# Kernel tuning notes

Measured on AMD Instinct MI355X. Metric: run time of the kernel, lower is better.

Reference implementation:

```python
import jax, jax.numpy as jnp
import numpy as np

B, S, D = 8, 512, 256
H, DH = 8, 32          # attention_heads, head_dim = 256/8
NB = 8                 # n_attention_blocks
COMP = 128             # compressed_features_size
LN_EPS = 1e-5


def _layernorm(x, g, b):
    mu = jnp.mean(x, axis=-1, keepdims=True)
    var = jnp.var(x, axis=-1, keepdims=True)
    return (x - mu) * jax.lax.rsqrt(var + LN_EPS) * g + b


def setup_inputs() -> dict:
    key = jax.random.key(0)
    ks = jax.random.split(key, 16)
    sc = 0.02
    d = {
        "state": jax.random.normal(ks[0], (B, S, 1, 64, 64), jnp.float32),
        "fc1_w": jax.random.normal(ks[1], (4096, 4096), jnp.float32) * sc,
        "fc1_b": jnp.zeros((4096,), jnp.float32),
        "fc2_w": jax.random.normal(ks[2], (4096, 2048), jnp.float32) * sc,
        "fc2_b": jnp.zeros((2048,), jnp.float32),
        "fc3_w": jax.random.normal(ks[3], (2048, 1024), jnp.float32) * sc,
        "fc3_b": jnp.zeros((1024,), jnp.float32),
        "fc4_w": jax.random.normal(ks[4], (1024, 512), jnp.float32) * sc,
        "fc4_b": jnp.zeros((512,), jnp.float32),
        "fc5_w": jax.random.normal(ks[5], (512, D), jnp.float32) * sc,
        "fc5_b": jnp.zeros((D,), jnp.float32),
        "pre_w": jax.random.normal(ks[6], (D, D), jnp.float32) * sc,
        "pre_b": jnp.zeros((D,), jnp.float32),
        "pos_w": jax.random.normal(ks[7], (1, S, D), jnp.float32) * sc,
        "enc_w": jax.random.normal(ks[8], (NB, D, 3 * D), jnp.float32) * sc,
        "enc_b": jnp.zeros((NB, 3 * D), jnp.float32),
        "ln1_g": jnp.ones((NB, D), jnp.float32),
        "ln1_b": jnp.zeros((NB, D), jnp.float32),
        "ln2_g": jnp.ones((NB, D), jnp.float32),
        "ln2_b": jnp.zeros((NB, D), jnp.float32),
        "res_w1": jax.random.normal(ks[9], (NB, D, 4 * D), jnp.float32) * sc,
        "res_b1": jnp.zeros((NB, 4 * D), jnp.float32),
        "res_w2": jax.random.normal(ks[10], (NB, 4 * D, D), jnp.float32) * sc,
        "res_b2": jnp.zeros((NB, D), jnp.float32),
        "out_w": jax.random.normal(ks[11], (D, COMP), jnp.float32) * sc,
        "out_b": jnp.zeros((COMP,), jnp.float32),
    }
    return d


def _forward(state, fc1_w, fc1_b, fc2_w, fc2_b, fc3_w, fc3_b, fc4_w, fc4_b,
             fc5_w, fc5_b, pre_w, pre_b, pos_w, enc_w, enc_b,
             ln1_g, ln1_b, ln2_g, ln2_b, res_w1, res_b1, res_w2, res_b2,
             out_w, out_b):
    x = state.reshape(B, S, -1)                       # [B,S,4096]
    x = jax.nn.relu(x @ fc1_w + fc1_b)
    x = jax.nn.relu(x @ fc2_w + fc2_b)
    x = jax.nn.relu(x @ fc3_w + fc3_b)
    x = jax.nn.relu(x @ fc4_w + fc4_b)
    x = jnp.tanh(x @ fc5_w + fc5_b)                   # [B,S,256]
    x = x @ pre_w + pre_b
    x = x + pos_w                                     # positional (dropout off / eval)

    i = jnp.arange(S)[:, None]
    j = jnp.arange(S)[None, :]
    m = (i >= j).astype(jnp.float32)[None, None]      # causal mask [1,1,S,S]
    scale = jax.lax.rsqrt(jnp.float32(DH))

    for l in range(NB):
        xn = _layernorm(x, ln1_g[l], ln1_b[l])
        c = xn @ enc_w[l] + enc_b[l]                  # [B,S,3D]
        q, k, v = jnp.split(c, 3, axis=2)
        q = q.reshape(B, S, H, DH).transpose(0, 2, 1, 3)  # [B,H,S,DH]
        k = k.reshape(B, S, H, DH).transpose(0, 2, 1, 3)
        v = v.reshape(B, S, H, DH).transpose(0, 2, 1, 3)
        w = jnp.einsum("bhqd,bhkd->bhqk", q, k) * scale
        w = w * m - 1e10 * (1.0 - m)
        s = jax.nn.softmax(w, axis=3)
        a = jnp.einsum("bhqk,bhkd->bhqd", s, v)
        a = a.transpose(0, 2, 1, 3).reshape(B, S, D)
        x = x + a
        x = _layernorm(x, ln2_g[l], ln2_b[l])
        h = jax.nn.gelu(x @ res_w1[l] + res_b1[l], approximate=False)
        h = h @ res_w2[l] + res_b2[l]
        x = x + h

    enc = x @ out_w + out_b                           # [B,S,128]
    enc = (enc - jnp.mean(enc)) / jnp.std(enc, ddof=1) + 1e-10
    return enc


def reference(state, fc1_w, fc1_b, fc2_w, fc2_b, fc3_w, fc3_b, fc4_w, fc4_b,
              fc5_w, fc5_b, pre_w, pre_b, pos_w, enc_w, enc_b,
              ln1_g, ln1_b, ln2_g, ln2_b, res_w1, res_b1, res_w2, res_b2,
              out_w, out_b):
    return _forward(state, fc1_w, fc1_b, fc2_w, fc2_b, fc3_w, fc3_b, fc4_w,
                    fc4_b, fc5_w, fc5_b, pre_w, pre_b, pos_w, enc_w, enc_b,
                    ln1_g, ln1_b, ln2_g, ln2_b, res_w1, res_b1, res_w2,
                    res_b2, out_w, out_b)
```

## Files before the change

### kernel.cpp

```cpp
#include <hip/hip_runtime.h>

typedef _Float16 half8 __attribute__((ext_vector_type(8)));
typedef _Float16 half4v __attribute__((ext_vector_type(4)));
typedef _Float16 half2v __attribute__((ext_vector_type(2)));
typedef float f32x4 __attribute__((ext_vector_type(4)));

__device__ __forceinline__ void gload16(const _Float16* g, _Float16* l) {
  __builtin_amdgcn_global_load_lds((const __attribute__((address_space(1))) void*)g,
                                   (__attribute__((address_space(3))) void*)l, 16, 0, 0);
}

__global__ __launch_bounds__(256) void cast_k(const float* __restrict__ in,
                                              _Float16* __restrict__ out, int n) {
  int i = (blockIdx.x * 256 + threadIdx.x) << 2;
  if (i < n) {
    float4 v = *(const float4*)(in + i);
    half4v h;
    h[0] = (_Float16)v.x; h[1] = (_Float16)v.y; h[2] = (_Float16)v.z; h[3] = (_Float16)v.w;
    *(half4v*)(out + i) = h;
  }
}

__global__ __launch_bounds__(256) void tcast_k(const float* __restrict__ W,
                                               _Float16* __restrict__ WT, int K, int N) {
  __shared__ float tile[32][33];
  const size_t zo = (size_t)blockIdx.z * K * N;
  const int n0 = blockIdx.x << 5, k0 = blockIdx.y << 5;
  const int tx = threadIdx.x & 31, ty = threadIdx.x >> 5;
#pragma unroll
  for (int i = 0; i < 4; i++)
    tile[ty + i * 8][tx] = W[zo + (size_t)(k0 + ty + i * 8) * N + n0 + tx];
  __syncthreads();
#pragma unroll
  for (int i = 0; i < 4; i++)
    WT[zo + (size_t)(n0 + ty + i * 8) * K + k0 + tx] = (_Float16)tile[tx][ty + i * 8];
}

template <int BM, int BN, int WGM, int WGN, int MODE>
__global__ __launch_bounds__(256) void gemm_nt(const _Float16* __restrict__ A,
                                               const _Float16* __restrict__ Bt,
                                               const float* __restrict__ bias,
                                               _Float16* __restrict__ outH,
                                               float* __restrict__ outF,
                                               const float* __restrict__ aux,
                                               int M, int N, int K) {
  constexpr int BK = 64;
  constexpr int TM = BM / WGM, TN = BN / WGN;
  constexpr int AM = TM / 16, AN = TN / 16;
  constexpr int LA = BM * BK / 2048, LB = BN * BK / 2048;
  __shared__ __align__(16) _Float16 As[BM * BK];
  __shared__ __align__(16) _Float16 Bs[BN * BK];
  const int tid = threadIdx.x;
  const int lane = tid & 63, w = tid >> 6;
  const int wr = (w / WGN) * TM, wc = (w % WGN) * TN;
  const int lr = lane & 15, quad = lane >> 4;
  const int mb = blockIdx.y * BM, nb = blockIdx.x * BN;

  const _Float16* ga[LA];
  const _Float16* gb[LB];
  _Float16* la[LA];
  _Float16* lb[LB];
#pragma unroll
  for (int i = 0; i < LA; i++) {
    const int c = tid + i * 256, row = c >> 3, j = c & 7;
    ga[i] = A + (size_t)(mb + row) * K + ((j ^ (row & 7)) << 3);
    la[i] = As + c * 8;
  }
#pragma unroll
  for (int i = 0; i < LB; i++) {
    const int c = tid + i * 256, row = c >> 3, j = c & 7;
    gb[i] = Bt + (size_t)(nb + row) * K + ((j ^ (row & 7)) << 3);
    lb[i] = Bs + c * 8;
  }

  f32x4 acc[AM][AN] = {};

  for (int k0 = 0; k0 < K; k0 += BK) {
#pragma unroll
    for (int i = 0; i < LA; i++) gload16(ga[i] + k0, la[i]);
#pragma unroll
    for (int i = 0; i < LB; i++) gload16(gb[i] + k0, lb[i]);
    __syncthreads();
#pragma unroll
    for (int ks = 0; ks < 2; ks++) {
      const int pc = (((ks << 2) | quad) ^ (lane & 7)) << 3;
      half8 af[AM], bf[AN];
#pragma unroll
      for (int mt = 0; mt < AM; mt++)
        af[mt] = *(const half8*)(As + (wr + mt * 16 + lr) * BK + pc);
#pragma unroll
      for (int nt = 0; nt < AN; nt++)
        bf[nt] = *(const half8*)(Bs + (wc + nt * 16 + lr) * BK + pc);
#pragma unroll
      for (int mt = 0; mt < AM; mt++)
#pragma unroll
        for (int nt = 0; nt < AN; nt++)
          acc[mt][nt] = __builtin_amdgcn_mfma_f32_16x16x32_f16(af[mt], bf[nt], acc[mt][nt], 0, 0, 0);
    }
    __syncthreads();
  }

#pragma unroll
  for (int nt = 0; nt < AN; nt++) {
    const int col = nb + wc + (nt << 4) + lr;
    const float bv = bias[col];
#pragma unroll
    for (int mt = 0; mt < AM; mt++) {
      const int row0 = mb + wr + (mt << 4) + (quad << 2);
#pragma unroll
      for (int r = 0; r < 4; r++) {
        const int row = row0 + r;
        const size_t off = (size_t)row * N + col;
        float v = acc[mt][nt][r] + bv;
        if (MODE == 0) {
          outH[off] = (_Float16)fmaxf(v, 0.0f);
        } else if (MODE == 1) {
          outH[off] = (_Float16)tanhf(v);
        } else if (MODE == 2) {
          outH[off] = (_Float16)v;
        } else if (MODE == 3) {
          outF[off] = v + aux[(size_t)(row & 511) * N + col];
        } else if (MODE == 4) {
          outH[off] = (_Float16)(0.5f * v * (1.0f + erff(v * 0.70710678118654752f)));
        } else if (MODE == 5) {
          float xv = aux[off] + v;
          outF[off] = xv;
          outH[off] = (_Float16)xv;
        } else {
          outF[off] = v;
        }
      }
    }
  }
}

__global__ __launch_bounds__(256) void ln_k(const float* __restrict__ x,
                                            const float* __restrict__ g,
                                            const float* __restrict__ b,
                                            _Float16* __restrict__ xn) {
  const int w = threadIdx.x >> 6, lane = threadIdx.x & 63;
  const int row = (blockIdx.x << 2) + w;
  const size_t base = ((size_t)row << 8) + (lane << 2);
  float4 v = *(const float4*)(x + base);
  float s = v.x + v.y + v.z + v.w;
  float sq = v.x * v.x + v.y * v.y + v.z * v.z + v.w * v.w;
#pragma unroll
  for (int o = 32; o; o >>= 1) { s += __shfl_xor(s, o); sq += __shfl_xor(sq, o); }
  const float mean = s * 0.00390625f;
  const float rs = rsqrtf(sq * 0.00390625f - mean * mean + 1e-5f);
  const int c = lane << 2;
  float4 gv = *(const float4*)(g + c);
  float4 bv = *(const float4*)(b + c);
  half4v o4;
  o4[0] = (_Float16)((v.x - mean) * rs * gv.x + bv.x);
  o4[1] = (_Float16)((v.y - mean) * rs * gv.y + bv.y);
  o4[2] = (_Float16)((v.z - mean) * rs * gv.z + bv.z);
  o4[3] = (_Float16)((v.w - mean) * rs * gv.w + bv.w);
  *(half4v*)(xn + base) = o4;
}

__global__ __launch_bounds__(256) void add_ln_k(const float* __restrict__ x,
                                                const float* __restrict__ a,
                                                const float* __restrict__ g,
                                                const float* __restrict__ b,
                                                float* __restrict__ xo,
                                                _Float16* __restrict__ xn) {
  const int w = threadIdx.x >> 6, lane = threadIdx.x & 63;
  const int row = (blockIdx.x << 2) + w;
  const size_t base = ((size_t)row << 8) + (lane << 2);
  float4 v = *(const float4*)(x + base);
  float4 av = *(const float4*)(a + base);
  v.x += av.x; v.y += av.y; v.z += av.z; v.w += av.w;
  float s = v.x + v.y + v.z + v.w;
  float sq = v.x * v.x + v.y * v.y + v.z * v.z + v.w * v.w;
#pragma unroll
  for (int o = 32; o; o >>= 1) { s += __shfl_xor(s, o); sq += __shfl_xor(sq, o); }
  const float mean = s * 0.00390625f;
  const float rs = rsqrtf(sq * 0.00390625f - mean * mean + 1e-5f);
  const int c = lane << 2;
  float4 gv = *(const float4*)(g + c);
  float4 bv = *(const float4*)(b + c);
  float4 o4;
  o4.x = (v.x - mean) * rs * gv.x + bv.x;
  o4.y = (v.y - mean) * rs * gv.y + bv.y;
  o4.z = (v.z - mean) * rs * gv.z + bv.z;
  o4.w = (v.w - mean) * rs * gv.w + bv.w;
  *(float4*)(xo + base) = o4;
  half4v h;
  h[0] = (_Float16)o4.x; h[1] = (_Float16)o4.y; h[2] = (_Float16)o4.z; h[3] = (_Float16)o4.w;
  *(half4v*)(xn + base) = h;
}

__global__ __launch_bounds__(256) void attn_k(const _Float16* __restrict__ qkv,
                                              float* __restrict__ aout) {
  __shared__ __align__(16) char smem[65536];
  _Float16* Ks = (_Float16*)smem;
  _Float16* Vs = (_Float16*)(smem + 32768);
  float* Om = (float*)smem;
  float* Ol = (float*)(smem + 768);
  float* Os = (float*)(smem + 1536);

  const int bid = blockIdx.x;
  const int qt = 7 - (bid & 7), h = (bid >> 3) & 7, b = bid >> 6;
  const int q0 = qt << 6;
  const int t = threadIdx.x, p = t >> 6, tr = t & 63, q = q0 + tr;
  const int nkt = qt + 1;
  const size_t rowbase = (size_t)(b * 512) * 768;

  const half2v* q2 = (const half2v*)(qkv + rowbase + (size_t)q * 768 + h * 32);
  half2v qh[16];
#pragma unroll
  for (int i = 0; i < 16; i++) qh[i] = q2[i];

  for (int c = t; c < nkt * 256; c += 256) {
    const int row = c >> 2, off = (c & 3) << 3;
    const _Float16* kp = qkv + rowbase + (size_t)row * 768 + 256 + h * 32 + off;
    gload16(kp, Ks + c * 8);
    gload16(kp + 256, Vs + c * 8);
  }
  __syncthreads();

  float O[32];
#pragma unroll
  for (int d = 0; d < 32; d++) O[d] = 0.0f;
  float m = -1e30f, lsum = 0.0f;

  for (int kt = p; kt < nkt; kt += 4) {
    const int kb = kt << 6;
    const int rows = (kt == qt) ? (tr + 1) : 64;
    for (int j0 = 0; j0 < rows; j0 += 8) {
      float s[8];
      float mx = -1e30f;
#pragma unroll
      for (int jj = 0; jj < 8; jj++) {
        const half2v* kr = (const half2v*)(Ks + (size_t)(kb + j0 + jj) * 32);
        float a0 = 0.0f, a1 = 0.0f;
#pragma unroll
        for (int d = 0; d < 8; d++) {
          a0 = __builtin_amdgcn_fdot2(qh[d], kr[d], a0, false);
          a1 = __builtin_amdgcn_fdot2(qh[d + 8], kr[d + 8], a1, false);
        }
        const float sc = (a0 + a1) * 0.17677669529663687f;
        s[jj] = (kb + j0 + jj <= q) ? sc : -1e30f;
        mx = fmaxf(mx, s[jj]);
      }
      const float mn = fmaxf(m, mx);
      const float corr = __expf(m - mn);
      lsum *= corr;
#pragma unroll
      for (int d = 0; d < 32; d++) O[d] *= corr;
      m = mn;
#pragma unroll
      for (int jj = 0; jj < 8; jj++) {
        const float pw = __expf(s[jj] - m);
        lsum += pw;
        const half8* vr = (const half8*)(Vs + (size_t)(kb + j0 + jj) * 32);
#pragma unroll
        for (int i = 0; i < 4; i++) {
          half8 vv = vr[i];
#pragma unroll
          for (int d = 0; d < 8; d++) O[i * 8 + d] = fmaf(pw, (float)vv[d], O[i * 8 + d]);
        }
      }
    }
  }

  __syncthreads();
  if (p > 0) {
    Om[(p - 1) * 64 + tr] = m;
    Ol[(p - 1) * 64 + tr] = lsum;
    float* od = Os + ((p - 1) * 64 + tr) * 33;
#pragma unroll
    for (int d = 0; d < 32; d++) od[d] = O[d];
  }
  __syncthreads();
  if (p == 0) {
    float mn = m;
#pragma unroll
    for (int pp = 0; pp < 3; pp++) mn = fmaxf(mn, Om[pp * 64 + tr]);
    const float c0 = __expf(m - mn);
    float lt = lsum * c0;
    float cs[3];
#pragma unroll
    for (int pp = 0; pp < 3; pp++) {
      cs[pp] = __expf(Om[pp * 64 + tr] - mn);
      lt += Ol[pp * 64 + tr] * cs[pp];
    }
    const float inv = 1.0f / lt;
    float* op = aout + ((size_t)(b * 512 + q)) * 256 + h * 32;
#pragma unroll
    for (int d = 0; d < 32; d++) {
      float v = O[d] * c0;
#pragma unroll
      for (int pp = 0; pp < 3; pp++) v += Os[(pp * 64 + tr) * 33 + d] * cs[pp];
      op[d] = v * inv;
    }
  }
}

__global__ __launch_bounds__(256) void reduce_stats_k(const float4* __restrict__ v, int n4,
                                                      float* __restrict__ stats) {
  float s = 0.0f, sq = 0.0f;
  for (int i = blockIdx.x * 256 + threadIdx.x; i < n4; i += gridDim.x * 256) {
    float4 x = v[i];
    s += x.x + x.y + x.z + x.w;
    sq += x.x * x.x + x.y * x.y + x.z * x.z + x.w * x.w;
  }
#pragma unroll
  for (int o = 32; o; o >>= 1) { s += __shfl_xor(s, o); sq += __shfl_xor(sq, o); }
  __shared__ float ss[4], sqq[4];
  const int w = threadIdx.x >> 6;
  if ((threadIdx.x & 63) == 0) { ss[w] = s; sqq[w] = sq; }
  __syncthreads();
  if (threadIdx.x == 0) {
    atomicAdd(&stats[0], ss[0] + ss[1] + ss[2] + ss[3]);
    atomicAdd(&stats[1], sqq[0] + sqq[1] + sqq[2] + sqq[3]);
  }
}

__global__ __launch_bounds__(256) void finalize_k(const float4* __restrict__ enc,
                                                  const float* __restrict__ stats,
                                                  float4* __restrict__ out, int n4, float n) {
  const int i = blockIdx.x * 256 + threadIdx.x;
  if (i >= n4) return;
  const float s = stats[0], q = stats[1];
  const float mean = s / n;
  const float var = (q - s * s / n) / (n - 1.0f);
  const float inv = rsqrtf(var);
  float4 x = enc[i];
  float4 o;
  o.x = (x.x - mean) * inv + 1e-10f;
  o.y = (x.y - mean) * inv + 1e-10f;
  o.z = (x.z - mean) * inv + 1e-10f;
  o.w = (x.w - mean) * inv + 1e-10f;
  out[i] = o;
}

extern "C" void kernel_launch(void* const* d_in, const int* in_sizes, int n_in,
                              void* d_out, int out_size, void* d_ws, size_t ws_size,
                              hipStream_t stream) {
  const float* state = (const float*)d_in[0];
  const float* fc1_w = (const float*)d_in[1];
  const float* fc1_b = (const float*)d_in[2];
  const float* fc2_w = (const float*)d_in[3];
  const float* fc2_b = (const float*)d_in[4];
  const float* fc3_w = (const float*)d_in[5];
  const float* fc3_b = (const float*)d_in[6];
  const float* fc4_w = (const float*)d_in[7];
  const float* fc4_b = (const float*)d_in[8];
  const float* fc5_w = (const float*)d_in[9];
  const float* fc5_b = (const float*)d_in[10];
  const float* pre_w = (const float*)d_in[11];
  const float* pre_b = (const float*)d_in[12];
  const float* pos_w = (const float*)d_in[13];
  const float* enc_w = (const float*)d_in[14];
  const float* enc_b = (const float*)d_in[15];
  const float* ln1_g = (const float*)d_in[16];
  const float* ln1_b = (const float*)d_in[17];
  const float* ln2_g = (const float*)d_in[18];
  const float* ln2_b = (const float*)d_in[19];
  const float* res_w1 = (const float*)d_in[20];
  const float* res_b1 = (const float*)d_in[21];
  const float* res_w2 = (const float*)d_in[22];
  const float* res_b2 = (const float*)d_in[23];
  const float* out_w = (const float*)d_in[24];
  const float* out_b = (const float*)d_in[25];

  char* ws = (char*)d_ws;
  _Float16* wbuf = (_Float16*)ws;
  _Float16* bufA = (_Float16*)(ws + 33554432);
  _Float16* bufB = (_Float16*)(ws + 67108864);
  _Float16* xn16 = bufA;
  _Float16* qkv16 = bufA + 1048576;
  _Float16* h16 = bufA + 4194304;
  _Float16* x16 = bufA + 8388608;
  float* xres = (float*)(ws + 67108864 + 4194304);
  float* aout = xres + 1048576;
  float* enc32 = aout + 1048576;
  float* stats = enc32 + 524288;
  _Float16* encT = (_Float16*)(ws + 67108864 + 16777216);
  _Float16* res1T = encT + 1572864;
  _Float16* res2T = res1T + 2097152;
  _Float16* outT = res2T + 2097152;

  const dim3 tb(256);

  cast_k<<<16384, tb, 0, stream>>>(state, bufA, 16777216);
  tcast_k<<<dim3(128, 128, 1), tb, 0, stream>>>(fc1_w, wbuf, 4096, 4096);
  gemm_nt<128, 128, 2, 2, 0><<<dim3(32, 32), tb, 0, stream>>>(bufA, wbuf, fc1_b, bufB, nullptr, nullptr, 4096, 4096, 4096);
  tcast_k<<<dim3(64, 128, 1), tb, 0, stream>>>(fc2_w, wbuf, 4096, 2048);
  gemm_nt<128, 128, 2, 2, 0><<<dim3(16, 32), tb, 0, stream>>>(bufB, wbuf, fc2_b, bufA, nullptr, nullptr, 4096, 2048, 4096);
  tcast_k<<<dim3(32, 64, 1), tb, 0, stream>>>(fc3_w, wbuf, 2048, 1024);
  gemm_nt<128, 128, 2, 2, 0><<<dim3(8, 32), tb, 0, stream>>>(bufA, wbuf, fc3_b, bufB, nullptr, nullptr, 4096, 1024, 2048);
  tcast_k<<<dim3(16, 32, 1), tb, 0, stream>>>(fc4_w, wbuf, 1024, 512);
  gemm_nt<128, 64, 4, 1, 0><<<dim3(8, 32), tb, 0, stream>>>(bufB, wbuf, fc4_b, bufA, nullptr, nullptr, 4096, 512, 1024);
  tcast_k<<<dim3(8, 16, 1), tb, 0, stream>>>(fc5_w, wbuf, 512, 256);
  gemm_nt<64, 64, 2, 2, 1><<<dim3(4, 64), tb, 0, stream>>>(bufA, wbuf, fc5_b, bufB, nullptr, nullptr, 4096, 256, 512);
  tcast_k<<<dim3(8, 8, 1), tb, 0, stream>>>(pre_w, wbuf, 256, 256);
  gemm_nt<64, 64, 2, 2, 3><<<dim3(4, 64), tb, 0, stream>>>(bufB, wbuf, pre_b, nullptr, xres, pos_w, 4096, 256, 256);

  tcast_k<<<dim3(24, 8, 8), tb, 0, stream>>>(enc_w, encT, 256, 768);
  tcast_k<<<dim3(32, 8, 8), tb, 0, stream>>>(res_w1, res1T, 256, 1024);
  tcast_k<<<dim3(8, 32, 8), tb, 0, stream>>>(res_w2, res2T, 1024, 256);
  tcast_k<<<dim3(4, 8, 1), tb, 0, stream>>>(out_w, outT, 256, 128);

  for (int l = 0; l < 8; l++) {
    ln_k<<<1024, tb, 0, stream>>>(xres, ln1_g + l * 256, ln1_b + l * 256, xn16);
    gemm_nt<128, 64, 4, 1, 2><<<dim3(12, 32), tb, 0, stream>>>(xn16, encT + (size_t)l * 196608, enc_b + l * 768,
                                                               qkv16, nullptr, nullptr, 4096, 768, 256);
    attn_k<<<512, tb, 0, stream>>>(qkv16, aout);
    add_ln_k<<<1024, tb, 0, stream>>>(xres, aout, ln2_g + l * 256, ln2_b + l * 256, xres, xn16);
    gemm_nt<128, 128, 2, 2, 4><<<dim3(8, 32), tb, 0, stream>>>(xn16, res1T + (size_t)l * 262144, res_b1 + l * 1024,
                                                               h16, nullptr, nullptr, 4096, 1024, 256);
    gemm_nt<64, 64, 2, 2, 5><<<dim3(4, 64), tb, 0, stream>>>(h16, res2T + (size_t)l * 262144, res_b2 + l * 256,
                                                             x16, xres, xres, 4096, 256, 1024);
  }

  gemm_nt<64, 64, 2, 2, 6><<<dim3(2, 64), tb, 0, stream>>>(x16, outT, out_b, nullptr, enc32, nullptr, 4096, 128, 256);
  hipMemsetAsync(stats, 0, 2 * sizeof(float), stream);
  reduce_stats_k<<<256, tb, 0, stream>>>((const float4*)enc32, 131072, stats);
  finalize_k<<<512, tb, 0, stream>>>((const float4*)enc32, stats, (float4*)d_out, 131072, 524288.0f);
}
```

Baseline: 1.438 ms.

## Fuse layernorms into GEMMs, merge weight casts, fold stats into output GEMM

Replaces the separate ln_k and add_ln_k kernels with a gemm_ln kernel that computes the (residual add +) layernorm of a 64-row tile in registers, writes fp16 into LDS, and runs the K=256 GEMM directly. The residual buffer is ping-ponged so the fused kernel can write the normalized residual while other blocks still read the old one. The four transformer weight transpose-casts are merged into one launch, the global mean/std reduction is folded into the final GEMM via atomics, and BK is made a template parameter with new tile shapes for the fc3–fc5, pre and res2 GEMMs. Each gemm_ln block recomputes the layernorm for its rows (once per column block), trading extra reads for fewer launches and round trips.

Measured after the change: 1.719 ms. 1.2x slower.

```diff
diff --git a/kernel.cpp b/kernel.cpp
--- a/kernel.cpp
+++ b/kernel.cpp
@@ -21,30 +21,61 @@
   }
 }
 
+__device__ __forceinline__ void tcast_core(const float* __restrict__ W,
+                                           _Float16* __restrict__ WT, int K, int N,
+                                           int n0, int k0, float tile[32][33]) {
+  const int tx = threadIdx.x & 31, ty = threadIdx.x >> 5;
+#pragma unroll
+  for (int i = 0; i < 4; i++)
+    tile[ty + i * 8][tx] = W[(size_t)(k0 + ty + i * 8) * N + n0 + tx];
+  __syncthreads();
+#pragma unroll
+  for (int i = 0; i < 4; i++)
+    WT[(size_t)(n0 + ty + i * 8) * K + k0 + tx] = (_Float16)tile[tx][ty + i * 8];
+}
+
 __global__ __launch_bounds__(256) void tcast_k(const float* __restrict__ W,
                                                _Float16* __restrict__ WT, int K, int N) {
   __shared__ float tile[32][33];
-  const size_t zo = (size_t)blockIdx.z * K * N;
-  const int n0 = blockIdx.x << 5, k0 = blockIdx.y << 5;
-  const int tx = threadIdx.x & 31, ty = threadIdx.x >> 5;
-#pragma unroll
-  for (int i = 0; i < 4; i++)
-    tile[ty + i * 8][tx] = W[zo + (size_t)(k0 + ty + i * 8) * N + n0 + tx];
-  __syncthreads();
-#pragma unroll
-  for (int i = 0; i < 4; i++)
-    WT[zo + (size_t)(n0 + ty + i * 8) * K + k0 + tx] = (_Float16)tile[tx][ty + i * 8];
-}
-
-template <int BM, int BN, int WGM, int WGN, int MODE>
+  tcast_core(W, WT, K, N, blockIdx.x << 5, blockIdx.y << 5, tile);
+}
+
+__global__ __launch_bounds__(256) void tcast_all(const float* __restrict__ enc_w, _Float16* encT,
+                                                 const float* __restrict__ res_w1, _Float16* res1T,
+                                                 const float* __restrict__ res_w2, _Float16* res2T,
+                                                 const float* __restrict__ out_w, _Float16* outT) {
+  __shared__ float tile[32][33];
+  int bid = blockIdx.x;
+  if (bid < 1536) {
+    const int z = bid / 192, r = bid % 192;
+    tcast_core(enc_w + (size_t)z * 196608, encT + (size_t)z * 196608, 256, 768,
+               (r % 24) << 5, (r / 24) << 5, tile);
+  } else if (bid < 3584) {
+    bid -= 1536;
+    const int z = bid / 256, r = bid % 256;
+    tcast_core(res_w1 + (size_t)z * 262144, res1T + (size_t)z * 262144, 256, 1024,
+               (r % 32) << 5, (r / 32) << 5, tile);
+  } else if (bid < 5632) {
+    bid -= 3584;
+    const int z = bid / 256, r = bid % 256;
+    tcast_core(res_w2 + (size_t)z * 262144, res2T + (size_t)z * 262144, 1024, 256,
+               (r % 8) << 5, (r / 8) << 5, tile);
+  } else {
+    bid -= 5632;
+    tcast_core(out_w, outT, 256, 128, (bid % 4) << 5, (bid / 4) << 5, tile);
+  }
+}
+
+template <int BM, int BN, int BK, int WGM, int WGN, int MODE>
 __global__ __launch_bounds__(256) void gemm_nt(const _Float16* __restrict__ A,
                                                const _Float16* __restrict__ Bt,
                                                const float* __restrict__ bias,
                                                _Float16* __restrict__ outH,
                                                float* __restrict__ outF,
                                                const float* __restrict__ aux,
+                                               float* __restrict__ stats,
                                                int M, int N, int K) {
-  constexpr int BK = 64;
+  constexpr int CPR = BK / 8;
   constexpr int TM = BM / WGM, TN = BN / WGN;
   constexpr int AM = TM / 16, AN = TN / 16;
   constexpr int LA = BM * BK / 2048, LB = BN * BK / 2048;
@@ -62,13 +93,13 @@
   _Float16* lb[LB];
 #pragma unroll
   for (int i = 0; i < LA; i++) {
-    const int c = tid + i * 256, row = c >> 3, j = c & 7;
+    const int c = tid + i * 256, row = c / CPR, j = c % CPR;
     ga[i] = A + (size_t)(mb + row) * K + ((j ^ (row & 7)) << 3);
     la[i] = As + c * 8;
   }
 #pragma unroll
   for (int i = 0; i < LB; i++) {
-    const int c = tid + i * 256, row = c >> 3, j = c & 7;
+    const int c = tid + i * 256, row = c / CPR, j = c % CPR;
     gb[i] = Bt + (size_t)(nb + row) * K + ((j ^ (row & 7)) << 3);
     lb[i] = Bs + c * 8;
   }
@@ -82,7 +113,7 @@
     for (int i = 0; i < LB; i++) gload16(gb[i] + k0, lb[i]);
     __syncthreads();
 #pragma unroll
-    for (int ks = 0; ks < 2; ks++) {
+    for (int ks = 0; ks < BK / 32; ks++) {
       const int pc = (((ks << 2) | quad) ^ (lane & 7)) << 3;
       half8 af[AM], bf[AN];
 #pragma unroll
@@ -100,6 +131,7 @@
     __syncthreads();
   }
 
+  float ls = 0.0f, lsq = 0.0f;
 #pragma unroll
   for (int nt = 0; nt < AN; nt++) {
     const int col = nb + wc + (nt << 4) + lr;
@@ -128,67 +160,128 @@
           outH[off] = (_Float16)xv;
         } else {
           outF[off] = v;
+          if (MODE == 7) { ls += v; lsq += v * v; }
         }
       }
     }
   }
-}
-
-__global__ __launch_bounds__(256) void ln_k(const float* __restrict__ x,
-                                            const float* __restrict__ g,
-                                            const float* __restrict__ b,
-                                            _Float16* __restrict__ xn) {
-  const int w = threadIdx.x >> 6, lane = threadIdx.x & 63;
-  const int row = (blockIdx.x << 2) + w;
-  const size_t base = ((size_t)row << 8) + (lane << 2);
-  float4 v = *(const float4*)(x + base);
-  float s = v.x + v.y + v.z + v.w;
-  float sq = v.x * v.x + v.y * v.y + v.z * v.z + v.w * v.w;
-#pragma unroll
-  for (int o = 32; o; o >>= 1) { s += __shfl_xor(s, o); sq += __shfl_xor(sq, o); }
-  const float mean = s * 0.00390625f;
-  const float rs = rsqrtf(sq * 0.00390625f - mean * mean + 1e-5f);
-  const int c = lane << 2;
-  float4 gv = *(const float4*)(g + c);
-  float4 bv = *(const float4*)(b + c);
-  half4v o4;
-  o4[0] = (_Float16)((v.x - mean) * rs * gv.x + bv.x);
-  o4[1] = (_Float16)((v.y - mean) * rs * gv.y + bv.y);
-  o4[2] = (_Float16)((v.z - mean) * rs * gv.z + bv.z);
-  o4[3] = (_Float16)((v.w - mean) * rs * gv.w + bv.w);
-  *(half4v*)(xn + base) = o4;
-}
-
-__global__ __launch_bounds__(256) void add_ln_k(const float* __restrict__ x,
-                                                const float* __restrict__ a,
-                                                const float* __restrict__ g,
-                                                const float* __restrict__ b,
-                                                float* __restrict__ xo,
-                                                _Float16* __restrict__ xn) {
-  const int w = threadIdx.x >> 6, lane = threadIdx.x & 63;
-  const int row = (blockIdx.x << 2) + w;
-  const size_t base = ((size_t)row << 8) + (lane << 2);
-  float4 v = *(const float4*)(x + base);
-  float4 av = *(const float4*)(a + base);
-  v.x += av.x; v.y += av.y; v.z += av.z; v.w += av.w;
-  float s = v.x + v.y + v.z + v.w;
-  float sq = v.x * v.x + v.y * v.y + v.z * v.z + v.w * v.w;
-#pragma unroll
-  for (int o = 32; o; o >>= 1) { s += __shfl_xor(s, o); sq += __shfl_xor(sq, o); }
-  const float mean = s * 0.00390625f;
-  const float rs = rsqrtf(sq * 0.00390625f - mean * mean + 1e-5f);
-  const int c = lane << 2;
-  float4 gv = *(const float4*)(g + c);
-  float4 bv = *(const float4*)(b + c);
-  float4 o4;
-  o4.x = (v.x - mean) * rs * gv.x + bv.x;
-  o4.y = (v.y - mean) * rs * gv.y + bv.y;
-  o4.z = (v.z - mean) * rs * gv.z + bv.z;
-  o4.w = (v.w - mean) * rs * gv.w + bv.w;
-  *(float4*)(xo + base) = o4;
-  half4v h;
-  h[0] = (_Float16)o4.x; h[1] = (_Float16)o4.y; h[2] = (_Float16)o4.z; h[3] = (_Float16)o4.w;
-  *(half4v*)(xn + base) = h;
+  if (MODE == 7) {
+#pragma unroll
+    for (int o = 32; o; o >>= 1) { ls += __shfl_xor(ls, o); lsq += __shfl_xor(lsq, o); }
+    if (lane == 0) {
+      atomicAdd(&stats[0], ls);
+      atomicAdd(&stats[1], lsq);
+    }
+  }
+}
+
+template <int MODE, bool ADD>
+__global__ __launch_bounds__(256) void gemm_ln(const float* __restrict__ X,
+                                               const float* __restrict__ Aadd,
+                                               const float* __restrict__ lng,
+                                               const float* __restrict__ lnb,
+                                               const _Float16* __restrict__ Bt,
+                                               const float* __restrict__ bias,
+                                               _Float16* __restrict__ outH,
+                                               float* __restrict__ xout, int N) {
+  __shared__ __align__(16) _Float16 As[64 * 256];
+  __shared__ __align__(16) _Float16 Bs[64 * 256];
+  const int tid = threadIdx.x;
+  const int lane = tid & 63, w = tid >> 6;
+  const int wr = (w >> 1) << 5, wc = (w & 1) << 5;
+  const int lr = lane & 15, quad = lane >> 4;
+  const int mb = blockIdx.y << 6, nb = blockIdx.x << 6;
+
+#pragma unroll
+  for (int i = 0; i < 8; i++) {
+    const int c = tid + i * 256, row = c >> 5, j = c & 31;
+    gload16(Bt + (size_t)(nb + row) * 256 + ((j ^ (row & 7)) << 3), Bs + c * 8);
+  }
+
+  const int r = tid >> 2, qq = tid & 3;
+  float vals[64];
+  {
+    const float4* xp = (const float4*)(X + ((size_t)(mb + r) << 8) + (qq << 6));
+    const float4* ap = (const float4*)(Aadd + ((size_t)(mb + r) << 8) + (qq << 6));
+    float s = 0.0f, sq = 0.0f;
+#pragma unroll
+    for (int i = 0; i < 16; i++) {
+      float4 v = xp[i];
+      if (ADD) {
+        float4 a = ap[i];
+        v.x += a.x; v.y += a.y; v.z += a.z; v.w += a.w;
+      }
+      vals[i * 4 + 0] = v.x; vals[i * 4 + 1] = v.y; vals[i * 4 + 2] = v.z; vals[i * 4 + 3] = v.w;
+      s += v.x + v.y + v.z + v.w;
+      sq += v.x * v.x + v.y * v.y + v.z * v.z + v.w * v.w;
+    }
+    s += __shfl_xor(s, 1); s += __shfl_xor(s, 2);
+    sq += __shfl_xor(sq, 1); sq += __shfl_xor(sq, 2);
+    const float mean = s * 0.00390625f;
+    const float rs = rsqrtf(sq * 0.00390625f - mean * mean + 1e-5f);
+    const float4* g4 = (const float4*)(lng + (qq << 6));
+    const float4* b4 = (const float4*)(lnb + (qq << 6));
+#pragma unroll
+    for (int i = 0; i < 16; i++) {
+      float4 g = g4[i], b = b4[i];
+      vals[i * 4 + 0] = (vals[i * 4 + 0] - mean) * rs * g.x + b.x;
+      vals[i * 4 + 1] = (vals[i * 4 + 1] - mean) * rs * g.y + b.y;
+      vals[i * 4 + 2] = (vals[i * 4 + 2] - mean) * rs * g.z + b.z;
+      vals[i * 4 + 3] = (vals[i * 4 + 3] - mean) * rs * g.w + b.w;
+    }
+#pragma unroll
+    for (int cc = 0; cc < 8; cc++) {
+      half8 h;
+#pragma unroll
+      for (int j = 0; j < 8; j++) h[j] = (_Float16)vals[cc * 8 + j];
+      *(half8*)(As + r * 256 + ((((qq << 3) | cc) ^ (r & 7)) << 3)) = h;
+    }
+    if (ADD && blockIdx.x == 0) {
+      float4* xo = (float4*)(xout + ((size_t)(mb + r) << 8) + (qq << 6));
+#pragma unroll
+      for (int i = 0; i < 16; i++) {
+        float4 o;
+        o.x = vals[i * 4 + 0]; o.y = vals[i * 4 + 1]; o.z = vals[i * 4 + 2]; o.w = vals[i * 4 + 3];
+        xo[i] = o;
+      }
+    }
+  }
+  __syncthreads();
+
+  f32x4 acc[2][2] = {};
+#pragma unroll
+  for (int ks = 0; ks < 8; ks++) {
+    const int pc = (((ks << 2) | quad) ^ (lane & 7)) << 3;
+    half8 af[2], bf[2];
+#pragma unroll
+    for (int mt = 0; mt < 2; mt++) af[mt] = *(const half8*)(As + (wr + mt * 16 + lr) * 256 + pc);
+#pragma unroll
+    for (int nt = 0; nt < 2; nt++) bf[nt] = *(const half8*)(Bs + (wc + nt * 16 + lr) * 256 + pc);
+#pragma unroll
+    for (int mt = 0; mt < 2; mt++)
+#pragma unroll
+      for (int nt = 0; nt < 2; nt++)
+        acc[mt][nt] = __builtin_amdgcn_mfma_f32_16x16x32_f16(af[mt], bf[nt], acc[mt][nt], 0, 0, 0);
+  }
+
+#pragma unroll
+  for (int nt = 0; nt < 2; nt++) {
+    const int col = nb + wc + (nt << 4) + lr;
+    const float bv = bias[col];
+#pragma unroll
+    for (int mt = 0; mt < 2; mt++) {
+      const int row0 = mb + wr + (mt << 4) + (quad << 2);
+#pragma unroll
+      for (int rr = 0; rr < 4; rr++) {
+        const size_t off = (size_t)(row0 + rr) * N + col;
+        float v = acc[mt][nt][rr] + bv;
+        if (MODE == 4)
+          outH[off] = (_Float16)(0.5f * v * (1.0f + erff(v * 0.70710678118654752f)));
+        else
+          outH[off] = (_Float16)v;
+      }
+    }
+  }
 }
 
 __global__ __launch_bounds__(256) void attn_k(const _Float16* __restrict__ qkv,
@@ -295,26 +388,6 @@
       for (int pp = 0; pp < 3; pp++) v += Os[(pp * 64 + tr) * 33 + d] * cs[pp];
       op[d] = v * inv;
     }
-  }
-}
-
-__global__ __launch_bounds__(256) void reduce_stats_k(const float4* __restrict__ v, int n4,
-                                                      float* __restrict__ stats) {
-  float s = 0.0f, sq = 0.0f;
-  for (int i = blockIdx.x * 256 + threadIdx.x; i < n4; i += gridDim.x * 256) {
-    float4 x = v[i];
-    s += x.x + x.y + x.z + x.w;
-    sq += x.x * x.x + x.y * x.y + x.z * x.z + x.w * x.w;
-  }
-#pragma unroll
-  for (int o = 32; o; o >>= 1) { s += __shfl_xor(s, o); sq += __shfl_xor(sq, o); }
-  __shared__ float ss[4], sqq[4];
-  const int w = threadIdx.x >> 6;
-  if ((threadIdx.x & 63) == 0) { ss[w] = s; sqq[w] = sq; }
-  __syncthreads();
-  if (threadIdx.x == 0) {
-    atomicAdd(&stats[0], ss[0] + ss[1] + ss[2] + ss[3]);
-    atomicAdd(&stats[1], sqq[0] + sqq[1] + sqq[2] + sqq[3]);
   }
 }
 
@@ -369,16 +442,16 @@
   char* ws = (char*)d_ws;
   _Float16* wbuf = (_Float16*)ws;
   _Float16* bufA = (_Float16*)(ws + 33554432);
-  _Float16* bufB = (_Float16*)(ws + 67108864);
-  _Float16* xn16 = bufA;
+  char* bufB = ws + 67108864;
   _Float16* qkv16 = bufA + 1048576;
   _Float16* h16 = bufA + 4194304;
   _Float16* x16 = bufA + 8388608;
-  float* xres = (float*)(ws + 67108864 + 4194304);
-  float* aout = xres + 1048576;
-  float* enc32 = aout + 1048576;
-  float* stats = enc32 + 524288;
-  _Float16* encT = (_Float16*)(ws + 67108864 + 16777216);
+  float* xres = (float*)(bufB + 4194304);
+  float* aout = (float*)(bufB + 8388608);
+  float* xres2 = (float*)(bufB + 12582912);
+  float* enc32 = (float*)(bufB + 16777216);
+  float* stats = (float*)(bufB + 18874368);
+  _Float16* encT = (_Float16*)(bufB + 20971520);
   _Float16* res1T = encT + 1572864;
   _Float16* res2T = res1T + 2097152;
   _Float16* outT = res2T + 2097152;
@@ -386,38 +459,34 @@
   const dim3 tb(256);
 
   cast_k<<<16384, tb, 0, stream>>>(state, bufA, 16777216);
-  tcast_k<<<dim3(128, 128, 1), tb, 0, stream>>>(fc1_w, wbuf, 4096, 4096);
-  gemm_nt<128, 128, 2, 2, 0><<<dim3(32, 32), tb, 0, stream>>>(bufA, wbuf, fc1_b, bufB, nullptr, nullptr, 4096, 4096, 4096);
-  tcast_k<<<dim3(64, 128, 1), tb, 0, stream>>>(fc2_w, wbuf, 4096, 2048);
-  gemm_nt<128, 128, 2, 2, 0><<<dim3(16, 32), tb, 0, stream>>>(bufB, wbuf, fc2_b, bufA, nullptr, nullptr, 4096, 2048, 4096);
-  tcast_k<<<dim3(32, 64, 1), tb, 0, stream>>>(fc3_w, wbuf, 2048, 1024);
-  gemm_nt<128, 128, 2, 2, 0><<<dim3(8, 32), tb, 0, stream>>>(bufA, wbuf, fc3_b, bufB, nullptr, nullptr, 4096, 1024, 2048);
-  tcast_k<<<dim3(16, 32, 1), tb, 0, stream>>>(fc4_w, wbuf, 1024, 512);
-  gemm_nt<128, 64, 4, 1, 0><<<dim3(8, 32), tb, 0, stream>>>(bufB, wbuf, fc4_b, bufA, nullptr, nullptr, 4096, 512, 1024);
-  tcast_k<<<dim3(8, 16, 1), tb, 0, stream>>>(fc5_w, wbuf, 512, 256);
-  gemm_nt<64, 64, 2, 2, 1><<<dim3(4, 64), tb, 0, stream>>>(bufA, wbuf, fc5_b, bufB, nullptr, nullptr, 4096, 256, 512);
-  tcast_k<<<dim3(8, 8, 1), tb, 0, stream>>>(pre_w, wbuf, 256, 256);
-  gemm_nt<64, 64, 2, 2, 3><<<dim3(4, 64), tb, 0, stream>>>(bufB, wbuf, pre_b, nullptr, xres, pos_w, 4096, 256, 256);
-
-  tcast_k<<<dim3(24, 8, 8), tb, 0, stream>>>(enc_w, encT, 256, 768);
-  tcast_k<<<dim3(32, 8, 8), tb, 0, stream>>>(res_w1, res1T, 256, 1024);
-  tcast_k<<<dim3(8, 32, 8), tb, 0, stream>>>(res_w2, res2T, 1024, 256);
-  tcast_k<<<dim3(4, 8, 1), tb, 0, stream>>>(out_w, outT, 256, 128);
+  tcast_k<<<dim3(128, 128), tb, 0, stream>>>(fc1_w, wbuf, 4096, 4096);
+  gemm_nt<128, 128, 64, 2, 2, 0><<<dim3(32, 32), tb, 0, stream>>>(bufA, wbuf, fc1_b, (_Float16*)bufB, nullptr, nullptr, nullptr, 4096, 4096, 4096);
+  tcast_k<<<dim3(64, 128), tb, 0, stream>>>(fc2_w, wbuf, 4096, 2048);
+  gemm_nt<128, 128, 64, 2, 2, 0><<<dim3(16, 32), tb, 0, stream>>>((_Float16*)bufB, wbuf, fc2_b, bufA, nullptr, nullptr, nullptr, 4096, 2048, 4096);
+  tcast_k<<<dim3(32, 64), tb, 0, stream>>>(fc3_w, wbuf, 2048, 1024);
+  gemm_nt<128, 64, 64, 2, 2, 0><<<dim3(16, 32), tb, 0, stream>>>(bufA, wbuf, fc3_b, (_Float16*)bufB, nullptr, nullptr, nullptr, 4096, 1024, 2048);
+  tcast_k<<<dim3(16, 32), tb, 0, stream>>>(fc4_w, wbuf, 1024, 512);
+  gemm_nt<64, 64, 128, 2, 2, 0><<<dim3(8, 64), tb, 0, stream>>>((_Float16*)bufB, wbuf, fc4_b, bufA, nullptr, nullptr, nullptr, 4096, 512, 1024);
+  tcast_k<<<dim3(8, 16), tb, 0, stream>>>(fc5_w, wbuf, 512, 256);
+  gemm_nt<64, 64, 256, 2, 2, 1><<<dim3(4, 64), tb, 0, stream>>>(bufA, wbuf, fc5_b, (_Float16*)bufB, nullptr, nullptr, nullptr, 4096, 256, 512);
+  tcast_k<<<dim3(8, 8), tb, 0, stream>>>(pre_w, wbuf, 256, 256);
+  gemm_nt<64, 64, 256, 2, 2, 3><<<dim3(4, 64), tb, 0, stream>>>((_Float16*)bufB, wbuf, pre_b, nullptr, xres, pos_w, nullptr, 4096, 256, 256);
+
+  tcast_all<<<5664, tb, 0, stream>>>(enc_w, encT, res_w1, res1T, res_w2, res2T, out_w, outT);
 
   for (int l = 0; l < 8; l++) {
-    ln_k<<<1024, tb, 0, stream>>>(xres, ln1_g + l * 256, ln1_b + l * 256, xn16);
-    gemm_nt<128, 64, 4, 1, 2><<<dim3(12, 32), tb, 0, stream>>>(xn16, encT + (size_t)l * 196608, enc_b + l * 768,
-                                                               qkv16, nullptr, nullptr, 4096, 768, 256);
+    float* R = (l & 1) ? xres2 : xres;
+    float* S = (l & 1) ? xres : xres2;
+    gemm_ln<2, false><<<dim3(12, 64), tb, 0, stream>>>(R, nullptr, ln1_g + l * 256, ln1_b + l * 256,
+                                                       encT + (size_t)l * 196608, enc_b + l * 768, qkv16, nullptr, 768);
     attn_k<<<512, tb, 0, stream>>>(qkv16, aout);
-    add_ln_k<<<1024, tb, 0, stream>>>(xres, aout, ln2_g + l * 256, ln2_b + l * 256, xres, xn16);
-    gemm_nt<128, 128, 2, 2, 4><<<dim3(8, 32), tb, 0, stream>>>(xn16, res1T + (size_t)l * 262144, res_b1 + l * 1024,
-                                                               h16, nullptr, nullptr, 4096, 1024, 256);
-    gemm_nt<64, 64, 2, 2, 5><<<dim3(4, 64), tb, 0, stream>>>(h16, res2T + (size_t)l * 262144, res_b2 + l * 256,
-                                                             x16, xres, xres, 4096, 256, 1024);
-  }
-
-  gemm_nt<64, 64, 2, 2, 6><<<dim3(2, 64), tb, 0, stream>>>(x16, outT, out_b, nullptr, enc32, nullptr, 4096, 128, 256);
+    gemm_ln<4, true><<<dim3(16, 64), tb, 0, stream>>>(R, aout, ln2_g + l * 256, ln2_b + l * 256,
+                                                      res1T + (size_t)l * 262144, res_b1 + l * 1024, h16, S, 1024);
+    gemm_nt<64, 64, 128, 2, 2, 5><<<dim3(4, 64), tb, 0, stream>>>(h16, res2T + (size_t)l * 262144, res_b2 + l * 256,
+                                                                  x16, S, S, nullptr, 4096, 256, 1024);
+  }
+
   hipMemsetAsync(stats, 0, 2 * sizeof(float), stream);
-  reduce_stats_k<<<256, tb, 0, stream>>>((const float4*)enc32, 131072, stats);
+  gemm_nt<64, 64, 256, 2, 2, 7><<<dim3(2, 64), tb, 0, stream>>>(x16, outT, out_b, nullptr, enc32, nullptr, stats, 4096, 128, 256);
   finalize_k<<<512, tb, 0, stream>>>((const float4*)enc32, stats, (float4*)d_out, 131072, 524288.0f);
 }
```

## Batch weight transposes into one kernel, fuse output stats, vectorize attention dots

Applied to the files above, without the earlier changes.

Replaces the many per-weight transpose-cast launches with a wider 64-column transpose kernel, plus one combined launch that converts all remaining weights into separate buffers. Fuses the sum and sum-of-squares reduction for the final normalization into the output GEMM epilogue using per-wave atomics, which drops the separate reduce kernel. Loads Q as half8 vectors in attention and splits the QK dot product across four accumulators. The GEMM now takes BK as a template parameter, though every call still uses 64. The cost is a larger workspace layout and float atomics whose summation order is nondeterministic.

Result: no change. 1.452 ms (+1.0%).

```diff
diff --git a/kernel.cpp b/kernel.cpp
--- a/kernel.cpp
+++ b/kernel.cpp
@@ -21,30 +21,68 @@
   }
 }
 
-__global__ __launch_bounds__(256) void tcast_k(const float* __restrict__ W,
-                                               _Float16* __restrict__ WT, int K, int N) {
-  __shared__ float tile[32][33];
-  const size_t zo = (size_t)blockIdx.z * K * N;
-  const int n0 = blockIdx.x << 5, k0 = blockIdx.y << 5;
-  const int tx = threadIdx.x & 31, ty = threadIdx.x >> 5;
-#pragma unroll
-  for (int i = 0; i < 4; i++)
-    tile[ty + i * 8][tx] = W[zo + (size_t)(k0 + ty + i * 8) * N + n0 + tx];
+__device__ __forceinline__ void t2core(const float* __restrict__ W, _Float16* __restrict__ WT,
+                                       int K, int N, int n0, int k0, float (*tile)[65]) {
+  const int tid = threadIdx.x;
+  const int n = tid & 63, kq = tid >> 6;
+#pragma unroll
+  for (int i = 0; i < 8; i++)
+    tile[kq * 8 + i][n] = W[(size_t)(k0 + kq * 8 + i) * N + n0 + n];
   __syncthreads();
-#pragma unroll
-  for (int i = 0; i < 4; i++)
-    WT[zo + (size_t)(n0 + ty + i * 8) * K + k0 + tx] = (_Float16)tile[tx][ty + i * 8];
-}
-
-template <int BM, int BN, int WGM, int WGN, int MODE>
+  const int nn = tid >> 2, c = tid & 3;
+  half8 h;
+#pragma unroll
+  for (int j = 0; j < 8; j++) h[j] = (_Float16)tile[c * 8 + j][nn];
+  *(half8*)(WT + (size_t)(n0 + nn) * K + k0 + c * 8) = h;
+}
+
+__global__ __launch_bounds__(256) void t2_k(const float* __restrict__ W,
+                                            _Float16* __restrict__ WT, int K, int N) {
+  __shared__ float tile[32][65];
+  t2core(W, WT, K, N, blockIdx.x << 6, blockIdx.y << 5, tile);
+}
+
+__global__ __launch_bounds__(256) void tcast_comb(
+    const float* __restrict__ fc2_w, _Float16* fc2T,
+    const float* __restrict__ fc3_w, _Float16* fc3T,
+    const float* __restrict__ fc4_w, _Float16* fc4T,
+    const float* __restrict__ fc5_w, _Float16* fc5T,
+    const float* __restrict__ pre_w, _Float16* preT,
+    const float* __restrict__ enc_w, _Float16* encT,
+    const float* __restrict__ res_w1, _Float16* res1T,
+    const float* __restrict__ res_w2, _Float16* res2T,
+    const float* __restrict__ out_w, _Float16* outT) {
+  __shared__ float tile[32][65];
+  int b = blockIdx.x;
+  const float* W; _Float16* WT; int K, N, n0, k0;
+  if (b < 4096)               { W = fc2_w; WT = fc2T; K = 4096; N = 2048; n0 = (b & 31) << 6; k0 = (b >> 5) << 5; }
+  else if ((b -= 4096) < 1024){ W = fc3_w; WT = fc3T; K = 2048; N = 1024; n0 = (b & 15) << 6; k0 = (b >> 4) << 5; }
+  else if ((b -= 1024) < 256) { W = fc4_w; WT = fc4T; K = 1024; N = 512;  n0 = (b & 7) << 6;  k0 = (b >> 3) << 5; }
+  else if ((b -= 256) < 64)   { W = fc5_w; WT = fc5T; K = 512;  N = 256;  n0 = (b & 3) << 6;  k0 = (b >> 2) << 5; }
+  else if ((b -= 64) < 32)    { W = pre_w; WT = preT; K = 256;  N = 256;  n0 = (b & 3) << 6;  k0 = (b >> 2) << 5; }
+  else if ((b -= 32) < 768)   { int z = b / 96, r = b % 96;
+                                W = enc_w + (size_t)z * 196608; WT = encT + (size_t)z * 196608;
+                                K = 256; N = 768; n0 = (r % 12) << 6; k0 = (r / 12) << 5; }
+  else if ((b -= 768) < 1024) { int z = b >> 7, r = b & 127;
+                                W = res_w1 + (size_t)z * 262144; WT = res1T + (size_t)z * 262144;
+                                K = 256; N = 1024; n0 = (r & 15) << 6; k0 = (r >> 4) << 5; }
+  else if ((b -= 1024) < 1024){ int z = b >> 7, r = b & 127;
+                                W = res_w2 + (size_t)z * 262144; WT = res2T + (size_t)z * 262144;
+                                K = 1024; N = 256; n0 = (r & 3) << 6; k0 = (r >> 2) << 5; }
+  else                        { b -= 1024; W = out_w; WT = outT; K = 256; N = 128; n0 = (b & 1) << 6; k0 = (b >> 1) << 5; }
+  t2core(W, WT, K, N, n0, k0, tile);
+}
+
+template <int BM, int BN, int BK, int WGM, int WGN, int MODE>
 __global__ __launch_bounds__(256) void gemm_nt(const _Float16* __restrict__ A,
                                                const _Float16* __restrict__ Bt,
                                                const float* __restrict__ bias,
                                                _Float16* __restrict__ outH,
                                                float* __restrict__ outF,
                                                const float* __restrict__ aux,
+                                               float* __restrict__ stats,
                                                int M, int N, int K) {
-  constexpr int BK = 64;
+  constexpr int CPR = BK / 8;
   constexpr int TM = BM / WGM, TN = BN / WGN;
   constexpr int AM = TM / 16, AN = TN / 16;
   constexpr int LA = BM * BK / 2048, LB = BN * BK / 2048;
@@ -62,13 +100,13 @@
   _Float16* lb[LB];
 #pragma unroll
   for (int i = 0; i < LA; i++) {
-    const int c = tid + i * 256, row = c >> 3, j = c & 7;
+    const int c = tid + i * 256, row = c / CPR, j = c % CPR;
     ga[i] = A + (size_t)(mb + row) * K + ((j ^ (row & 7)) << 3);
     la[i] = As + c * 8;
   }
 #pragma unroll
   for (int i = 0; i < LB; i++) {
-    const int c = tid + i * 256, row = c >> 3, j = c & 7;
+    const int c = tid + i * 256, row = c / CPR, j = c % CPR;
     gb[i] = Bt + (size_t)(nb + row) * K + ((j ^ (row & 7)) << 3);
     lb[i] = Bs + c * 8;
   }
@@ -82,7 +120,7 @@
     for (int i = 0; i < LB; i++) gload16(gb[i] + k0, lb[i]);
     __syncthreads();
 #pragma unroll
-    for (int ks = 0; ks < 2; ks++) {
+    for (int ks = 0; ks < BK / 32; ks++) {
       const int pc = (((ks << 2) | quad) ^ (lane & 7)) << 3;
       half8 af[AM], bf[AN];
 #pragma unroll
@@ -100,6 +138,7 @@
     __syncthreads();
   }
 
+  float ls = 0.0f, lsq = 0.0f;
 #pragma unroll
   for (int nt = 0; nt < AN; nt++) {
     const int col = nb + wc + (nt << 4) + lr;
@@ -128,8 +167,17 @@
           outH[off] = (_Float16)xv;
         } else {
           outF[off] = v;
+          if (MODE == 7) { ls += v; lsq += v * v; }
         }
       }
+    }
+  }
+  if (MODE == 7) {
+#pragma unroll
+    for (int o = 32; o; o >>= 1) { ls += __shfl_xor(ls, o); lsq += __shfl_xor(lsq, o); }
+    if (lane == 0) {
+      atomicAdd(&stats[0], ls);
+      atomicAdd(&stats[1], lsq);
     }
   }
 }
@@ -191,6 +239,17 @@
   *(half4v*)(xn + base) = h;
 }
 
+#define HP0(v) ((half2v)__builtin_shufflevector((v), (v), 0, 1))
+#define HP1(v) ((half2v)__builtin_shufflevector((v), (v), 2, 3))
+#define HP2(v) ((half2v)__builtin_shufflevector((v), (v), 4, 5))
+#define HP3(v) ((half2v)__builtin_shufflevector((v), (v), 6, 7))
+__device__ __forceinline__ float dot8(half8 a, half8 b, float acc) {
+  acc = __builtin_amdgcn_fdot2(HP0(a), HP0(b), acc, false);
+  acc = __builtin_amdgcn_fdot2(HP1(a), HP1(b), acc, false);
+  acc = __builtin_amdgcn_fdot2(HP2(a), HP2(b), acc, false);
+  acc = __builtin_amdgcn_fdot2(HP3(a), HP3(b), acc, false);
+  return acc;
+}
 __global__ __launch_bounds__(256) void attn_k(const _Float16* __restrict__ qkv,
                                               float* __restrict__ aout) {
   __shared__ __align__(16) char smem[65536];
@@ -207,10 +266,8 @@
   const int nkt = qt + 1;
   const size_t rowbase = (size_t)(b * 512) * 768;
 
-  const half2v* q2 = (const half2v*)(qkv + rowbase + (size_t)q * 768 + h * 32);
-  half2v qh[16];
-#pragma unroll
-  for (int i = 0; i < 16; i++) qh[i] = q2[i];
+  const half8* qr = (const half8*)(qkv + rowbase + (size_t)q * 768 + h * 32);
+  half8 qf0 = qr[0], qf1 = qr[1], qf2 = qr[2], qf3 = qr[3];
 
   for (int c = t; c < nkt * 256; c += 256) {
     const int row = c >> 2, off = (c & 3) << 3;
@@ -233,14 +290,13 @@
       float mx = -1e30f;
 #pragma unroll
       for (int jj = 0; jj < 8; jj++) {
-        const half2v* kr = (const half2v*)(Ks + (size_t)(kb + j0 + jj) * 32);
-        float a0 = 0.0f, a1 = 0.0f;
-#pragma unroll
-        for (int d = 0; d < 8; d++) {
-          a0 = __builtin_amdgcn_fdot2(qh[d], kr[d], a0, false);
-          a1 = __builtin_amdgcn_fdot2(qh[d + 8], kr[d + 8], a1, false);
-        }
-        const float sc = (a0 + a1) * 0.17677669529663687f;
+        const half8* kr = (const half8*)(Ks + (size_t)(kb + j0 + jj) * 32);
+        float a0 = 0.0f, a1 = 0.0f, a2 = 0.0f, a3 = 0.0f;
+        a0 = dot8(qf0, kr[0], a0);
+        a1 = dot8(qf1, kr[1], a1);
+        a2 = dot8(qf2, kr[2], a2);
+        a3 = dot8(qf3, kr[3], a3);
+        const float sc = ((a0 + a1) + (a2 + a3)) * 0.17677669529663687f;
         s[jj] = (kb + j0 + jj <= q) ? sc : -1e30f;
         mx = fmaxf(mx, s[jj]);
       }
@@ -295,26 +351,6 @@
       for (int pp = 0; pp < 3; pp++) v += Os[(pp * 64 + tr) * 33 + d] * cs[pp];
       op[d] = v * inv;
     }
-  }
-}
-
-__global__ __launch_bounds__(256) void reduce_stats_k(const float4* __restrict__ v, int n4,
-                                                      float* __restrict__ stats) {
-  float s = 0.0f, sq = 0.0f;
-  for (int i = blockIdx.x * 256 + threadIdx.x; i < n4; i += gridDim.x * 256) {
-    float4 x = v[i];
-    s += x.x + x.y + x.z + x.w;
-    sq += x.x * x.x + x.y * x.y + x.z * x.z + x.w * x.w;
-  }
-#pragma unroll
-  for (int o = 32; o; o >>= 1) { s += __shfl_xor(s, o); sq += __shfl_xor(sq, o); }
-  __shared__ float ss[4], sqq[4];
-  const int w = threadIdx.x >> 6;
-  if ((threadIdx.x & 63) == 0) { ss[w] = s; sqq[w] = sq; }
-  __syncthreads();
-  if (threadIdx.x == 0) {
-    atomicAdd(&stats[0], ss[0] + ss[1] + ss[2] + ss[3]);
-    atomicAdd(&stats[1], sqq[0] + sqq[1] + sqq[2] + sqq[3]);
   }
 }
 
@@ -368,56 +404,53 @@
 
   char* ws = (char*)d_ws;
   _Float16* wbuf = (_Float16*)ws;
-  _Float16* bufA = (_Float16*)(ws + 33554432);
-  _Float16* bufB = (_Float16*)(ws + 67108864);
-  _Float16* xn16 = bufA;
-  _Float16* qkv16 = bufA + 1048576;
-  _Float16* h16 = bufA + 4194304;
-  _Float16* x16 = bufA + 8388608;
-  float* xres = (float*)(ws + 67108864 + 4194304);
-  float* aout = xres + 1048576;
-  float* enc32 = aout + 1048576;
-  float* stats = enc32 + 524288;
-  _Float16* encT = (_Float16*)(ws + 67108864 + 16777216);
-  _Float16* res1T = encT + 1572864;
-  _Float16* res2T = res1T + 2097152;
-  _Float16* outT = res2T + 2097152;
+  _Float16* bufA16 = (_Float16*)(ws + (32 << 20));
+  char* bufB = ws + (64 << 20);
+
+  _Float16* fc2T = wbuf;
+  _Float16* fc3T = wbuf + 8388608;
+  _Float16* fc4T = wbuf + 10485760;
+  _Float16* encT = wbuf + 11010048;
+  _Float16* res1T = wbuf + 12582912;
+  _Float16* res2T = wbuf + 14680064;
+  _Float16* fc5T = bufA16 + 14680064;
+  _Float16* preT = bufA16 + 14811136;
+  _Float16* outT = bufA16 + 14876672;
+  _Float16* xn16 = bufA16;
+  _Float16* qkv16 = bufA16 + 1048576;
+  _Float16* h16 = bufA16 + 4194304;
+  _Float16* x16 = bufA16 + 8388608;
+  float* xres = (float*)(bufB + 8388608);
+  float* aout = (float*)(bufB + 12582912);
+  float* enc32 = (float*)(bufB + 20971520);
+  float* stats = (float*)(bufB + 23068672);
 
   const dim3 tb(256);
 
-  cast_k<<<16384, tb, 0, stream>>>(state, bufA, 16777216);
-  tcast_k<<<dim3(128, 128, 1), tb, 0, stream>>>(fc1_w, wbuf, 4096, 4096);
-  gemm_nt<128, 128, 2, 2, 0><<<dim3(32, 32), tb, 0, stream>>>(bufA, wbuf, fc1_b, bufB, nullptr, nullptr, 4096, 4096, 4096);
-  tcast_k<<<dim3(64, 128, 1), tb, 0, stream>>>(fc2_w, wbuf, 4096, 2048);
-  gemm_nt<128, 128, 2, 2, 0><<<dim3(16, 32), tb, 0, stream>>>(bufB, wbuf, fc2_b, bufA, nullptr, nullptr, 4096, 2048, 4096);
-  tcast_k<<<dim3(32, 64, 1), tb, 0, stream>>>(fc3_w, wbuf, 2048, 1024);
-  gemm_nt<128, 128, 2, 2, 0><<<dim3(8, 32), tb, 0, stream>>>(bufA, wbuf, fc3_b, bufB, nullptr, nullptr, 4096, 1024, 2048);
-  tcast_k<<<dim3(16, 32, 1), tb, 0, stream>>>(fc4_w, wbuf, 1024, 512);
-  gemm_nt<128, 64, 4, 1, 0><<<dim3(8, 32), tb, 0, stream>>>(bufB, wbuf, fc4_b, bufA, nullptr, nullptr, 4096, 512, 1024);
-  tcast_k<<<dim3(8, 16, 1), tb, 0, stream>>>(fc5_w, wbuf, 512, 256);
-  gemm_nt<64, 64, 2, 2, 1><<<dim3(4, 64), tb, 0, stream>>>(bufA, wbuf, fc5_b, bufB, nullptr, nullptr, 4096, 256, 512);
-  tcast_k<<<dim3(8, 8, 1), tb, 0, stream>>>(pre_w, wbuf, 256, 256);
-  gemm_nt<64, 64, 2, 2, 3><<<dim3(4, 64), tb, 0, stream>>>(bufB, wbuf, pre_b, nullptr, xres, pos_w, 4096, 256, 256);
-
-  tcast_k<<<dim3(24, 8, 8), tb, 0, stream>>>(enc_w, encT, 256, 768);
-  tcast_k<<<dim3(32, 8, 8), tb, 0, stream>>>(res_w1, res1T, 256, 1024);
-  tcast_k<<<dim3(8, 32, 8), tb, 0, stream>>>(res_w2, res2T, 1024, 256);
-  tcast_k<<<dim3(4, 8, 1), tb, 0, stream>>>(out_w, outT, 256, 128);
+  cast_k<<<16384, tb, 0, stream>>>(state, bufA16, 16777216);
+  t2_k<<<dim3(64, 128), tb, 0, stream>>>(fc1_w, wbuf, 4096, 4096);
+  gemm_nt<128, 128, 64, 2, 2, 0><<<dim3(32, 32), tb, 0, stream>>>(bufA16, wbuf, fc1_b, (_Float16*)bufB, nullptr, nullptr, nullptr, 4096, 4096, 4096);
+  tcast_comb<<<8304, tb, 0, stream>>>(fc2_w, fc2T, fc3_w, fc3T, fc4_w, fc4T, fc5_w, fc5T,
+                                      pre_w, preT, enc_w, encT, res_w1, res1T, res_w2, res2T, out_w, outT);
+  gemm_nt<128, 128, 64, 2, 2, 0><<<dim3(16, 32), tb, 0, stream>>>((_Float16*)bufB, fc2T, fc2_b, bufA16, nullptr, nullptr, nullptr, 4096, 2048, 4096);
+  gemm_nt<128, 128, 64, 2, 2, 0><<<dim3(8, 32), tb, 0, stream>>>(bufA16, fc3T, fc3_b, (_Float16*)bufB, nullptr, nullptr, nullptr, 4096, 1024, 2048);
+  gemm_nt<128, 64, 64, 4, 1, 0><<<dim3(8, 32), tb, 0, stream>>>((_Float16*)bufB, fc4T, fc4_b, bufA16, nullptr, nullptr, nullptr, 4096, 512, 1024);
+  gemm_nt<64, 64, 64, 2, 2, 1><<<dim3(4, 64), tb, 0, stream>>>(bufA16, fc5T, fc5_b, (_Float16*)bufB, nullptr, nullptr, nullptr, 4096, 256, 512);
+  gemm_nt<64, 64, 64, 2, 2, 3><<<dim3(4, 64), tb, 0, stream>>>((_Float16*)bufB, preT, pre_b, nullptr, xres, pos_w, nullptr, 4096, 256, 256);
 
   for (int l = 0; l < 8; l++) {
     ln_k<<<1024, tb, 0, stream>>>(xres, ln1_g + l * 256, ln1_b + l * 256, xn16);
-    gemm_nt<128, 64, 4, 1, 2><<<dim3(12, 32), tb, 0, stream>>>(xn16, encT + (size_t)l * 196608, enc_b + l * 768,
-                                                               qkv16, nullptr, nullptr, 4096, 768, 256);
+    gemm_nt<128, 64, 64, 4, 1, 2><<<dim3(12, 32), tb, 0, stream>>>(xn16, encT + (size_t)l * 196608, enc_b + l * 768,
+                                                                   qkv16, nullptr, nullptr, nullptr, 4096, 768, 256);
     attn_k<<<512, tb, 0, stream>>>(qkv16, aout);
     add_ln_k<<<1024, tb, 0, stream>>>(xres, aout, ln2_g + l * 256, ln2_b + l * 256, xres, xn16);
-    gemm_nt<128, 128, 2, 2, 4><<<dim3(8, 32), tb, 0, stream>>>(xn16, res1T + (size_t)l * 262144, res_b1 + l * 1024,
-                                                               h16, nullptr, nullptr, 4096, 1024, 256);
-    gemm_nt<64, 64, 2, 2, 5><<<dim3(4, 64), tb, 0, stream>>>(h16, res2T + (size_t)l * 262144, res_b2 + l * 256,
-                                                             x16, xres, xres, 4096, 256, 1024);
-  }
-
-  gemm_nt<64, 64, 2, 2, 6><<<dim3(2, 64), tb, 0, stream>>>(x16, outT, out_b, nullptr, enc32, nullptr, 4096, 128, 256);
-  hipMemsetAsync(stats, 0, 2 * sizeof(float), stream);
-  reduce_stats_k<<<256, tb, 0, stream>>>((const float4*)enc32, 131072, stats);
+    gemm_nt<128, 128, 64, 2, 2, 4><<<dim3(8, 32), tb, 0, stream>>>(xn16, res1T + (size_t)l * 262144, res_b1 + l * 1024,
+                                                                   h16, nullptr, nullptr, nullptr, 4096, 1024, 256);
+    gemm_nt<64, 64, 64, 2, 2, 5><<<dim3(4, 64), tb, 0, stream>>>(h16, res2T + (size_t)l * 262144, res_b2 + l * 256,
+                                                                 x16, xres, xres, nullptr, 4096, 256, 1024);
+  }
+
+  (void)hipMemsetAsync(stats, 0, 2 * sizeof(float), stream);
+  gemm_nt<64, 64, 64, 2, 2, 7><<<dim3(2, 64), tb, 0, stream>>>(x16, outT, out_b, nullptr, enc32, nullptr, stats, 4096, 128, 256);
   finalize_k<<<512, tb, 0, stream>>>((const float4*)enc32, stats, (float4*)d_out, 131072, 524288.0f);
 }
```
